# Kernel optimization log

Measured on AMD Instinct MI355X. Metric: run time of the kernel, lower is better.

The kernel has to match this reference:

```python
import jax, jax.numpy as jnp
import numpy as np

E = 1_600_000
NODE_D = 64
EDGE_D = 32
HIDDEN = 128
OUT_D = 32
IN_D = EDGE_D + 2 * NODE_D  # 160


def setup_inputs() -> dict:
    key = jax.random.key(0)
    ks = jax.random.split(key, 8)
    src = jax.random.normal(ks[0], (E, NODE_D), dtype=jnp.float32)
    dest = jax.random.normal(ks[1], (E, NODE_D), dtype=jnp.float32)
    edge_attr = jax.random.normal(ks[2], (E, EDGE_D), dtype=jnp.float32)
    u = jax.random.normal(ks[3], (16, 16), dtype=jnp.float32)
    batch = jax.random.randint(ks[4], (E,), 0, 16, dtype=jnp.int64)
    # MLP params: Linear(IN_D, HIDDEN) -> ReLU -> Linear(HIDDEN, OUT_D)
    w1 = jax.random.normal(ks[5], (IN_D, HIDDEN), dtype=jnp.float32) / np.sqrt(IN_D)
    b1 = jnp.zeros((HIDDEN,), dtype=jnp.float32)
    w2 = jax.random.normal(ks[6], (HIDDEN, OUT_D), dtype=jnp.float32) / np.sqrt(HIDDEN)
    b2 = jnp.zeros((OUT_D,), dtype=jnp.float32)
    return {"src": src, "dest": dest, "edge_attr": edge_attr, "u": u,
            "batch": batch, "w1": w1, "b1": b1, "w2": w2, "b2": b2}


def reference(src, dest, edge_attr, u, batch, w1, b1, w2, b2):
    # out = MLP(cat([src, dest, edge_attr], axis=1)); u, batch unused (MetaLayer API)
    x = jnp.concatenate([src, dest, edge_attr], axis=1)  # [E, IN_D]
    h = jax.nn.relu(x @ w1 + b1)                          # [E, HIDDEN]
    return h @ w2 + b2                                    # [E, OUT_D]
```

## Files before the change

### kernel.cpp

```cpp
#include <hip/hip_runtime.h>


typedef float  f32x4  __attribute__((ext_vector_type(4)));
typedef short  s16x8  __attribute__((ext_vector_type(8)));

__device__ __forceinline__ unsigned short f2bf(float f) {
    unsigned int u = __float_as_uint(f);
    u += 0x7FFFu + ((u >> 16) & 1u);
    return (unsigned short)(u >> 16);
}

__global__ __launch_bounds__(256, 2) void edge_mlp(
    const float* __restrict__ src, const float* __restrict__ dst,
    const float* __restrict__ edg, const float* __restrict__ w1,
    const float* __restrict__ b1, const float* __restrict__ w2,
    const float* __restrict__ b2, float* __restrict__ out, int ntiles)
{
    __shared__ __align__(16) unsigned short w1s[40 * 64 * 8];
    __shared__ __align__(16) unsigned short hbuf[4][16 * 128];

    const int t    = threadIdx.x;
    const int lane = t & 63;
    const int wid  = t >> 6;
    const int rq   = lane >> 4;
    const int rr   = lane & 15;

    for (int s = t; s < 40 * 64; s += 256) {
        const int f  = s >> 6, l = s & 63;
        const int kk = f >> 3, n = f & 7;
        const int k0 = kk * 32 + ((l >> 4) << 3);
        const int cl = (n << 4) + (l & 15);
        union { s16x8 v; unsigned short s16[8]; } r;
#pragma unroll
        for (int j = 0; j < 8; ++j)
            r.s16[j] = f2bf(w1[(k0 + j) * 128 + cl]);
        *reinterpret_cast<s16x8*>(&w1s[s * 8]) = r.v;
    }

    s16x8 w2f[4][2];
#pragma unroll
    for (int kk2 = 0; kk2 < 4; ++kk2)
#pragma unroll
        for (int n2 = 0; n2 < 2; ++n2) {
            union { s16x8 v; unsigned short s16[8]; } r;
#pragma unroll
            for (int j = 0; j < 8; ++j)
                r.s16[j] = f2bf(w2[(kk2 * 32 + (rq << 3) + j) * 32 + n2 * 16 + rr]);
            w2f[kk2][n2] = r.v;
        }
    float b1c[8], b2c[2];
#pragma unroll
    for (int n = 0; n < 8; ++n) b1c[n] = b1[n * 16 + rr];
#pragma unroll
    for (int n2 = 0; n2 < 2; ++n2) b2c[n2] = b2[n2 * 16 + rr];

    __syncthreads();

    unsigned short* hw = &hbuf[wid][0];

    for (int tile = blockIdx.x; tile < ntiles; tile += gridDim.x) {
        const size_t base = (size_t)tile * 128 + (size_t)wid * 32;

        f32x4 acc[2][8];
#pragma unroll
        for (int rf = 0; rf < 2; ++rf)
#pragma unroll
            for (int n = 0; n < 8; ++n)
                acc[rf][n] = (f32x4){b1c[n], b1c[n], b1c[n], b1c[n]};

#pragma unroll
        for (int kk = 0; kk < 5; ++kk) {
            const float* sp; int cols, cofs;
            if      (kk == 0) { sp = src; cols = 64; cofs = 0;  }
            else if (kk == 1) { sp = src; cols = 64; cofs = 32; }
            else if (kk == 2) { sp = dst; cols = 64; cofs = 0;  }
            else if (kk == 3) { sp = dst; cols = 64; cofs = 32; }
            else              { sp = edg; cols = 32; cofs = 0;  }

            s16x8 a[2];
#pragma unroll
            for (int rf = 0; rf < 2; ++rf) {
                const float* p = sp + (base + rf * 16 + rr) * cols + cofs + (rq << 3);
                f32x4 v0 = *reinterpret_cast<const f32x4*>(p);
                f32x4 v1 = *reinterpret_cast<const f32x4*>(p + 4);
                union { s16x8 v; unsigned short s16[8]; } r;
                r.s16[0] = f2bf(v0.x); r.s16[1] = f2bf(v0.y);
                r.s16[2] = f2bf(v0.z); r.s16[3] = f2bf(v0.w);
                r.s16[4] = f2bf(v1.x); r.s16[5] = f2bf(v1.y);
                r.s16[6] = f2bf(v1.z); r.s16[7] = f2bf(v1.w);
                a[rf] = r.v;
            }
#pragma unroll
            for (int n = 0; n < 8; ++n) {
                s16x8 b = *reinterpret_cast<const s16x8*>(&w1s[((kk * 8 + n) * 64 + lane) * 8]);
                acc[0][n] = __builtin_amdgcn_mfma_f32_16x16x32_bf16(a[0], b, acc[0][n], 0, 0, 0);
                acc[1][n] = __builtin_amdgcn_mfma_f32_16x16x32_bf16(a[1], b, acc[1][n], 0, 0, 0);
            }
        }

#pragma unroll
        for (int rf = 0; rf < 2; ++rf) {
#pragma unroll
            for (int n = 0; n < 8; ++n)
#pragma unroll
                for (int j = 0; j < 4; ++j) {
                    const int row  = rq * 4 + j;
                    const int addr = ((row * 256 + (n * 16 + rr) * 2) ^ ((row & 7) << 4));
                    float v = acc[rf][n][j];
                    v = v > 0.0f ? v : 0.0f;
                    *reinterpret_cast<unsigned short*>(
                        reinterpret_cast<char*>(hw) + addr) = f2bf(v);
                }
            asm volatile("" ::: "memory");

            f32x4 acc2[2];
#pragma unroll
            for (int n2 = 0; n2 < 2; ++n2)
                acc2[n2] = (f32x4){b2c[n2], b2c[n2], b2c[n2], b2c[n2]};

#pragma unroll
            for (int kk2 = 0; kk2 < 4; ++kk2) {
                const int row  = rr;
                const int addr = ((row * 256 + kk2 * 64 + rq * 16) ^ ((row & 7) << 4));
                s16x8 a2 = *reinterpret_cast<const s16x8*>(
                    reinterpret_cast<const char*>(hw) + addr);
                acc2[0] = __builtin_amdgcn_mfma_f32_16x16x32_bf16(a2, w2f[kk2][0], acc2[0], 0, 0, 0);
                acc2[1] = __builtin_amdgcn_mfma_f32_16x16x32_bf16(a2, w2f[kk2][1], acc2[1], 0, 0, 0);
            }
            asm volatile("" ::: "memory");

#pragma unroll
            for (int n2 = 0; n2 < 2; ++n2)
#pragma unroll
                for (int j = 0; j < 4; ++j) {
                    const size_t row = base + rf * 16 + rq * 4 + j;
                    out[row * 32 + n2 * 16 + rr] = acc2[n2][j];
                }
        }
    }
}

__global__ void edge_mlp_tail(
    const float* __restrict__ src, const float* __restrict__ dst,
    const float* __restrict__ edg, const float* __restrict__ w1,
    const float* __restrict__ b1, const float* __restrict__ w2,
    const float* __restrict__ b2, float* __restrict__ out,
    long long row0, long long E)
{
    const long long r = row0 + blockIdx.x;
    if (r >= E) return;
    __shared__ float h[128];
    const int t = threadIdx.x;
    float acc = b1[t];
    for (int k = 0; k < 64; ++k) acc += src[r * 64 + k] * w1[k * 128 + t];
    for (int k = 0; k < 64; ++k) acc += dst[r * 64 + k] * w1[(64 + k) * 128 + t];
    for (int k = 0; k < 32; ++k) acc += edg[r * 32 + k] * w1[(128 + k) * 128 + t];
    h[t] = acc > 0.0f ? acc : 0.0f;
    __syncthreads();
    if (t < 32) {
        float o = b2[t];
        for (int k = 0; k < 128; ++k) o += h[k] * w2[k * 32 + t];
        out[r * 32 + t] = o;
    }
}

extern "C" void kernel_launch(void* const* d_in, const int* in_sizes, int n_in,
                              void* d_out, int out_size, void* d_ws, size_t ws_size,
                              hipStream_t stream)
{
    const float* src = (const float*)d_in[0];
    const float* dst = (const float*)d_in[1];
    const float* edg = (const float*)d_in[2];
    const float* w1  = (const float*)d_in[5];
    const float* b1  = (const float*)d_in[6];
    const float* w2  = (const float*)d_in[7];
    const float* b2  = (const float*)d_in[8];
    float* out = (float*)d_out;

    const long long E      = (long long)in_sizes[0] / 64;
    const int       ntiles = (int)(E / 128);
    const long long rem    = E - (long long)ntiles * 128;

    if (ntiles > 0) {
        int grid = ntiles < 512 ? ntiles : 512;
        edge_mlp<<<dim3(grid), dim3(256), 0, stream>>>(
            src, dst, edg, w1, b1, w2, b2, out, ntiles);
    }
    if (rem > 0) {
        edge_mlp_tail<<<dim3((unsigned)rem), dim3(128), 0, stream>>>(
            src, dst, edg, w1, b1, w2, b2, out, (long long)ntiles * 128, E);
    }
}
```

Before: 248.6 us.

## Compute transposed first GEMM so hidden activations feed second MFMA from registers

The first MFMA swaps operands (weights as A, inputs as B) so each lane's accumulator holds hidden values in the layout the second MFMA needs as its A operand. W2 rows are permuted to match, and the LDS round trip for the hidden tile is removed. Blocks grow to 8 waves of 16 rows each at 512 threads, with b1 held in LDS. This removes the LDS stores and loads plus their swizzling, but halves the rows per wave, so there is less MFMA work to hide global load latency and register pressure changes under the new launch bounds.

```diff
diff --git a/kernel.cpp b/kernel.cpp
--- a/kernel.cpp
+++ b/kernel.cpp
@@ -10,14 +10,14 @@
     return (unsigned short)(u >> 16);
 }
 
-__global__ __launch_bounds__(256, 2) void edge_mlp(
+__global__ __launch_bounds__(512, 4) void edge_mlp(
     const float* __restrict__ src, const float* __restrict__ dst,
     const float* __restrict__ edg, const float* __restrict__ w1,
     const float* __restrict__ b1, const float* __restrict__ w2,
     const float* __restrict__ b2, float* __restrict__ out, int ntiles)
 {
     __shared__ __align__(16) unsigned short w1s[40 * 64 * 8];
-    __shared__ __align__(16) unsigned short hbuf[4][16 * 128];
+    __shared__ __align__(16) float b1s[128];
 
     const int t    = threadIdx.x;
     const int lane = t & 63;
@@ -25,48 +25,44 @@
     const int rq   = lane >> 4;
     const int rr   = lane & 15;
 
-    for (int s = t; s < 40 * 64; s += 256) {
+    for (int s = t; s < 40 * 64; s += 512) {
         const int f  = s >> 6, l = s & 63;
         const int kk = f >> 3, n = f & 7;
         const int k0 = kk * 32 + ((l >> 4) << 3);
         const int cl = (n << 4) + (l & 15);
-        union { s16x8 v; unsigned short s16[8]; } r;
+        union { s16x8 v; unsigned short u[8]; } r;
 #pragma unroll
         for (int j = 0; j < 8; ++j)
-            r.s16[j] = f2bf(w1[(k0 + j) * 128 + cl]);
+            r.u[j] = f2bf(w1[(k0 + j) * 128 + cl]);
         *reinterpret_cast<s16x8*>(&w1s[s * 8]) = r.v;
     }
+    if (t < 128) b1s[t] = b1[t];
 
     s16x8 w2f[4][2];
 #pragma unroll
-    for (int kk2 = 0; kk2 < 4; ++kk2)
+    for (int m = 0; m < 4; ++m)
 #pragma unroll
         for (int n2 = 0; n2 < 2; ++n2) {
-            union { s16x8 v; unsigned short s16[8]; } r;
+            union { s16x8 v; unsigned short u[8]; } r;
 #pragma unroll
-            for (int j = 0; j < 8; ++j)
-                r.s16[j] = f2bf(w2[(kk2 * 32 + (rq << 3) + j) * 32 + n2 * 16 + rr]);
-            w2f[kk2][n2] = r.v;
+            for (int j = 0; j < 4; ++j) {
+                r.u[j]     = f2bf(w2[(m * 16 + rq * 4 + j) * 32 + n2 * 16 + rr]);
+                r.u[4 + j] = f2bf(w2[((m + 4) * 16 + rq * 4 + j) * 32 + n2 * 16 + rr]);
+            }
+            w2f[m][n2] = r.v;
         }
-    float b1c[8], b2c[2];
-#pragma unroll
-    for (int n = 0; n < 8; ++n) b1c[n] = b1[n * 16 + rr];
-#pragma unroll
-    for (int n2 = 0; n2 < 2; ++n2) b2c[n2] = b2[n2 * 16 + rr];
+    const float b2c0 = b2[rr];
+    const float b2c1 = b2[16 + rr];
 
     __syncthreads();
 
-    unsigned short* hw = &hbuf[wid][0];
+    for (int tile = blockIdx.x; tile < ntiles; tile += gridDim.x) {
+        const size_t row0 = (size_t)tile * 128 + (size_t)wid * 16;
 
-    for (int tile = blockIdx.x; tile < ntiles; tile += gridDim.x) {
-        const size_t base = (size_t)tile * 128 + (size_t)wid * 32;
-
-        f32x4 acc[2][8];
+        f32x4 acc[8];
 #pragma unroll
-        for (int rf = 0; rf < 2; ++rf)
-#pragma unroll
-            for (int n = 0; n < 8; ++n)
-                acc[rf][n] = (f32x4){b1c[n], b1c[n], b1c[n], b1c[n]};
+        for (int n = 0; n < 8; ++n)
+            acc[n] = *reinterpret_cast<const f32x4*>(&b1s[n * 16 + rq * 4]);
 
 #pragma unroll
         for (int kk = 0; kk < 5; ++kk) {
@@ -77,66 +73,45 @@
             else if (kk == 3) { sp = dst; cols = 64; cofs = 32; }
             else              { sp = edg; cols = 32; cofs = 0;  }
 
-            s16x8 a[2];
-#pragma unroll
-            for (int rf = 0; rf < 2; ++rf) {
-                const float* p = sp + (base + rf * 16 + rr) * cols + cofs + (rq << 3);
-                f32x4 v0 = *reinterpret_cast<const f32x4*>(p);
-                f32x4 v1 = *reinterpret_cast<const f32x4*>(p + 4);
-                union { s16x8 v; unsigned short s16[8]; } r;
-                r.s16[0] = f2bf(v0.x); r.s16[1] = f2bf(v0.y);
-                r.s16[2] = f2bf(v0.z); r.s16[3] = f2bf(v0.w);
-                r.s16[4] = f2bf(v1.x); r.s16[5] = f2bf(v1.y);
-                r.s16[6] = f2bf(v1.z); r.s16[7] = f2bf(v1.w);
-                a[rf] = r.v;
-            }
+            const float* p = sp + (row0 + rr) * (size_t)cols + cofs + (rq << 3);
+            f32x4 v0 = *reinterpret_cast<const f32x4*>(p);
+            f32x4 v1 = *reinterpret_cast<const f32x4*>(p + 4);
+            union { s16x8 v; unsigned short u[8]; } a;
+            a.u[0] = f2bf(v0.x); a.u[1] = f2bf(v0.y);
+            a.u[2] = f2bf(v0.z); a.u[3] = f2bf(v0.w);
+            a.u[4] = f2bf(v1.x); a.u[5] = f2bf(v1.y);
+            a.u[6] = f2bf(v1.z); a.u[7] = f2bf(v1.w);
+
 #pragma unroll
             for (int n = 0; n < 8; ++n) {
-                s16x8 b = *reinterpret_cast<const s16x8*>(&w1s[((kk * 8 + n) * 64 + lane) * 8]);
-                acc[0][n] = __builtin_amdgcn_mfma_f32_16x16x32_bf16(a[0], b, acc[0][n], 0, 0, 0);
-                acc[1][n] = __builtin_amdgcn_mfma_f32_16x16x32_bf16(a[1], b, acc[1][n], 0, 0, 0);
+                s16x8 wv = *reinterpret_cast<const s16x8*>(&w1s[((kk * 8 + n) * 64 + lane) * 8]);
+                acc[n] = __builtin_amdgcn_mfma_f32_16x16x32_bf16(wv, a.v, acc[n], 0, 0, 0);
             }
         }
 
-#pragma unroll
-        for (int rf = 0; rf < 2; ++rf) {
-#pragma unroll
-            for (int n = 0; n < 8; ++n)
-#pragma unroll
-                for (int j = 0; j < 4; ++j) {
-                    const int row  = rq * 4 + j;
-                    const int addr = ((row * 256 + (n * 16 + rr) * 2) ^ ((row & 7) << 4));
-                    float v = acc[rf][n][j];
-                    v = v > 0.0f ? v : 0.0f;
-                    *reinterpret_cast<unsigned short*>(
-                        reinterpret_cast<char*>(hw) + addr) = f2bf(v);
-                }
-            asm volatile("" ::: "memory");
-
-            f32x4 acc2[2];
-#pragma unroll
-            for (int n2 = 0; n2 < 2; ++n2)
-                acc2[n2] = (f32x4){b2c[n2], b2c[n2], b2c[n2], b2c[n2]};
+        f32x4 acc2[2];
+        acc2[0] = (f32x4){b2c0, b2c0, b2c0, b2c0};
+        acc2[1] = (f32x4){b2c1, b2c1, b2c1, b2c1};
 
 #pragma unroll
-            for (int kk2 = 0; kk2 < 4; ++kk2) {
-                const int row  = rr;
-                const int addr = ((row * 256 + kk2 * 64 + rq * 16) ^ ((row & 7) << 4));
-                s16x8 a2 = *reinterpret_cast<const s16x8*>(
-                    reinterpret_cast<const char*>(hw) + addr);
-                acc2[0] = __builtin_amdgcn_mfma_f32_16x16x32_bf16(a2, w2f[kk2][0], acc2[0], 0, 0, 0);
-                acc2[1] = __builtin_amdgcn_mfma_f32_16x16x32_bf16(a2, w2f[kk2][1], acc2[1], 0, 0, 0);
+        for (int m = 0; m < 4; ++m) {
+            union { s16x8 v; unsigned short u[8]; } hh;
+#pragma unroll
+            for (int j = 0; j < 4; ++j) {
+                hh.u[j]     = f2bf(fmaxf(acc[m][j], 0.0f));
+                hh.u[4 + j] = f2bf(fmaxf(acc[m + 4][j], 0.0f));
             }
-            asm volatile("" ::: "memory");
+            acc2[0] = __builtin_amdgcn_mfma_f32_16x16x32_bf16(hh.v, w2f[m][0], acc2[0], 0, 0, 0);
+            acc2[1] = __builtin_amdgcn_mfma_f32_16x16x32_bf16(hh.v, w2f[m][1], acc2[1], 0, 0, 0);
+        }
 
 #pragma unroll
-            for (int n2 = 0; n2 < 2; ++n2)
+        for (int n2 = 0; n2 < 2; ++n2)
 #pragma unroll
-                for (int j = 0; j < 4; ++j) {
-                    const size_t row = base + rf * 16 + rq * 4 + j;
-                    out[row * 32 + n2 * 16 + rr] = acc2[n2][j];
-                }
-        }
+            for (int j = 0; j < 4; ++j) {
+                const size_t row = row0 + rq * 4 + j;
+                out[row * 32 + n2 * 16 + rr] = (n2 == 0 ? acc2[0][j] : acc2[1][j]);
+            }
     }
 }
 
@@ -183,7 +158,7 @@
 
     if (ntiles > 0) {
         int grid = ntiles < 512 ? ntiles : 512;
-        edge_mlp<<<dim3(grid), dim3(256), 0, stream>>>(
+        edge_mlp<<<dim3(grid), dim3(512), 0, stream>>>(
             src, dst, edg, w1, b1, w2, b2, out, ntiles);
     }
     if (rem > 0) {
```

Measured after the change: 912.6 us. 3.67x slower.
